# Optimization experiments

Measured on AMD Instinct MI355X. Metric: run time of the kernel, lower is better.

Reference implementation:

```python
import jax, jax.numpy as jnp
import numpy as np

RHO = 10.0
TAU = 0.1


def setup_inputs() -> dict:
    key = jax.random.key(0)
    k1, k2 = jax.random.split(key)
    N, D, C = 8192, 512, 128
    embeddings = jax.random.normal(k1, (N, D), dtype=jnp.float32)
    classes = jax.random.randint(k2, (N,), 0, C, dtype=jnp.int64)
    return {"embeddings": embeddings, "classes": classes}


def reference(embeddings, classes):
    n = embeddings.shape[0]
    dt = embeddings.dtype

    # calculate_similarities_pt: cosine similarity (dot products of L2-normalized embeddings)
    norms = jnp.linalg.norm(embeddings, axis=1, keepdims=True)
    normed = embeddings / jnp.maximum(norms, jnp.asarray(1e-12, dt))
    dot_products = jnp.einsum("nd,md->nm", normed, normed)  # [N, N]

    # calculate_groups_pt: same-class mask (excluding self) and different-class mask
    eq = classes[:, None] == classes[None, :]
    eye = jnp.eye(n, dtype=bool)
    same_group = (eq & ~eye).astype(dt)       # [N, N]
    different_group = (~eq).astype(dt)        # [N, N]

    # diagonal gets factor -RHO -> strongly negative score, effectively masked out
    raw_scores = ((same_group + different_group) * (1.0 + RHO) - RHO) * dot_products / TAU
    max_raw_score = jnp.max(raw_scores, axis=1, keepdims=True)
    shifted_scores = jnp.exp(raw_scores - max_raw_score)

    shifted_positive_scores = same_group * shifted_scores
    sum_shifted_negative_scores = jnp.sum(different_group * shifted_scores, axis=1, keepdims=True)

    denom = shifted_positive_scores + sum_shifted_negative_scores
    # safe_division: 0 where denominator is 0
    ratio = jnp.where(denom > 0, shifted_positive_scores / jnp.where(denom > 0, denom, 1.0), 0.0)
    # safe_log: 0 where argument is 0 (masked by same_group anyway)
    log_ratio = jnp.where(ratio > 0, jnp.log(jnp.where(ratio > 0, ratio, 1.0)), 0.0)
    infonce_losses = -log_ratio * same_group

    num_pos = jnp.sum(same_group)
    loss = jnp.where(num_pos > 0, jnp.sum(infonce_losses) / jnp.where(num_pos > 0, num_pos, 1.0), 0.0)
    return loss
```

## Files before the change

### kernel.cpp

```cpp
#include <hip/hip_runtime.h>
#include <hip/hip_bf16.h>


constexpr int   D      = 512;
constexpr int   BT     = 128;
constexpr int   BK     = 128;
constexpr int   NSTEP  = D / BK;
constexpr float SHIFTL = 14.4269504088896340f;
constexpr float QS2L   = 10.0f * 1.4426950408889634f / 16129.0f;
constexpr float LN2    = 0.6931471805599453f;

typedef __attribute__((ext_vector_type(4))) int i32x4;
typedef unsigned char uchar;
typedef unsigned long ulong_t;

__device__ inline void gload_lds16(const uchar* g, void* l) {
    __builtin_amdgcn_global_load_lds(
        (const __attribute__((address_space(1))) void*)g,
        (__attribute__((address_space(3))) void*)l, 16, 0, 0);
}

__global__ void k_normalize(const float* __restrict__ emb,
                            const int* __restrict__ classes,
                            uchar* __restrict__ normed,
                            int* __restrict__ hist, int n) {
    if (blockIdx.x == 0) {
        __shared__ int h[128];
        if (threadIdx.x < 128) h[threadIdx.x] = 0;
        __syncthreads();
        for (int i = threadIdx.x; i < n; i += 256)
            atomicAdd(&h[classes[i] & 127], 1);
        __syncthreads();
        if (threadIdx.x < 128) hist[threadIdx.x] = h[threadIdx.x];
    }
    int row  = blockIdx.x * 4 + (threadIdx.x >> 6);
    int lane = threadIdx.x & 63;
    if (row >= n) return;
    const float4* src = (const float4*)(emb + (size_t)row * D);
    float4 a = src[lane * 2];
    float4 b = src[lane * 2 + 1];
    float ss = a.x*a.x + a.y*a.y + a.z*a.z + a.w*a.w
             + b.x*b.x + b.y*b.y + b.z*b.z + b.w*b.w;
#pragma unroll
    for (int m = 1; m < 64; m <<= 1) ss += __shfl_xor(ss, m, 64);
    float sc = 127.0f / fmaxf(sqrtf(ss), 1e-12f);
    union { signed char c[8]; ulong_t u; } o;
    float v[8] = {a.x, a.y, a.z, a.w, b.x, b.y, b.z, b.w};
#pragma unroll
    for (int k = 0; k < 8; ++k) {
        int q = (int)rintf(v[k] * sc);
        q = q > 127 ? 127 : (q < -127 ? -127 : q);
        o.c[k] = (signed char)q;
    }
    *(ulong_t*)&normed[(size_t)row * D + lane * 8] = o.u;
}

__global__ __launch_bounds__(256, 2) void k_zgemm(
    const uchar* __restrict__ normed, const int* __restrict__ classes,
    float* __restrict__ Zpart, int n, int nb, int npairs) {
    __shared__ char ring[2][32768];
    __shared__ int clsrow[BT], clscol[BT];

    const int tid  = threadIdx.x;
    const int lane = tid & 63;
    const int w    = tid >> 6;
    const int wm   = w >> 1, wn = w & 1;
    const int l15  = lane & 15, l4 = lane >> 4;
    const size_t QS = (size_t)64 * n;

    int q8 = npairs >> 3, r8 = npairs & 7;
    int xcd = blockIdx.x & 7, off = blockIdx.x >> 3;
    int orig = (xcd < r8 ? xcd * (q8 + 1) : r8 * (q8 + 1) + (xcd - r8) * q8) + off;

    const int sgrid = nb >> 3;
    int idx = orig, si = 0;
    for (;;) { int rc = 36 + (sgrid - 1 - si) * 64; if (idx < rc) break; idx -= rc; ++si; }
    int bi, bj;
    if (idx < 36) { int u = 0, rem = 8; while (idx >= rem) { idx -= rem; ++u; --rem; }
                    bi = si * 8 + u; bj = si * 8 + u + idx; }
    else { idx -= 36; int sj = si + 1 + (idx >> 6); int v = idx & 63;
           bi = si * 8 + (v >> 3); bj = sj * 8 + (v & 7); }
    const int row0 = bi * BT, c0 = bj * BT;
    const bool diagblk = (bi == bj);

    if (tid < BT) clsrow[tid] = classes[row0 + tid];
    else          clscol[tid - BT] = classes[c0 + tid - BT];
    int crow[16];
#pragma unroll
    for (int t = 0; t < 16; ++t)
        crow[t] = classes[row0 + wm * 64 + (t >> 2) * 16 + l4 * 4 + (t & 3)];

    const int src16 = (lane & 3) ^ ((lane >> 3) & 3);
    size_t gA[2], gB[2]; int lo[2];
#pragma unroll
    for (int it = 0; it < 2; ++it) {
        int chunk = w * 2 + it;
        int row   = chunk * 16 + (lane >> 2);
        gA[it] = (size_t)(row0 + row) * D + src16 * 16;
        gB[it] = (size_t)(c0   + row) * D + src16 * 16;
        lo[it] = chunk * 1024;
    }
    char* ringb = &ring[0][0];

    auto STAGE = [&](int sbo, int kk) {
#pragma unroll
        for (int h = 0; h < 2; ++h) {
            int kh = kk + h * 64;
            int so = sbo + h * 16384;
#pragma unroll
            for (int it = 0; it < 2; ++it) {
                gload_lds16(normed + gA[it] + kh, ringb + so + lo[it]);
                gload_lds16(normed + gB[it] + kh, ringb + so + 8192 + lo[it]);
            }
        }
    };

    i32x4 acc[4][4];
#pragma unroll
    for (int a = 0; a < 4; ++a)
#pragma unroll
        for (int b = 0; b < 4; ++b) acc[a][b] = (i32x4){0, 0, 0, 0};

    STAGE(0, 0);
    __builtin_amdgcn_sched_barrier(0);
    asm volatile("s_waitcnt vmcnt(0) lgkmcnt(0)" ::: "memory");
    __builtin_amdgcn_s_barrier();
    __builtin_amdgcn_sched_barrier(0);

    const int rsw = (l15 >> 1) & 3;

#pragma unroll
    for (int kt = 0; kt < NSTEP; ++kt) {
        const int cur = kt & 1;
        if (kt + 1 < NSTEP) STAGE((cur ^ 1) * 32768, (kt + 1) * BK);
        const char* base = ringb + cur * 32768;
        i32x4 af[2][4], bfr[2][4];
#pragma unroll
        for (int h = 0; h < 2; ++h) {
            const char* la = base + h * 16384;
            const char* lb = la + 8192;
#pragma unroll
            for (int mf = 0; mf < 4; ++mf) {
                int ra = wm * 64 + mf * 16 + l15;
                af[h][mf] = *(const i32x4*)(la + ra * 64 + ((l4 ^ rsw) << 4));
            }
#pragma unroll
            for (int nf = 0; nf < 4; ++nf) {
                int rb = wn * 64 + nf * 16 + l15;
                bfr[h][nf] = *(const i32x4*)(lb + rb * 64 + ((l4 ^ rsw) << 4));
            }
        }
        __builtin_amdgcn_s_setprio(1);
#pragma unroll
        for (int h = 0; h < 2; ++h)
#pragma unroll
            for (int mf = 0; mf < 4; ++mf)
#pragma unroll
                for (int nf = 0; nf < 4; ++nf)
                    acc[mf][nf] = __builtin_amdgcn_mfma_i32_16x16x64_i8(
                        af[h][mf], bfr[h][nf], acc[mf][nf], 0, 0, 0);
        __builtin_amdgcn_s_setprio(0);
        __builtin_amdgcn_sched_barrier(0);
        if (kt + 1 < NSTEP) {
            asm volatile("s_waitcnt vmcnt(0)" ::: "memory");
            __builtin_amdgcn_s_barrier();
            __builtin_amdgcn_sched_barrier(0);
        }
    }
    __syncthreads();

    float cqz[4] = {0,0,0,0}, cqn[4] = {0,0,0,0}, cqp[4] = {0,0,0,0};
    float* redr = (float*)ringb;
    float* redc = (float*)(ringb + 16384);

#pragma unroll
    for (int mf = 0; mf < 4; ++mf) {
#pragma unroll
        for (int r = 0; r < 4; ++r) {
            int rr = wm * 64 + mf * 16 + l4 * 4 + r;
            int rg = row0 + rr;
            int cr = crow[mf * 4 + r];
            float z = 0.f, ns = 0.f, p1 = 0.f;
#pragma unroll
            for (int nf = 0; nf < 4; ++nf) {
                int cc = wn * 64 + nf * 16 + l15;
                float t = fmaf((float)acc[mf][nf][r], QS2L, -SHIFTL);
                float e = exp2f(t);
                bool same = (cr == clscol[cc]);
                bool dg   = (rg == c0 + cc);
                if (!same) { z += e; cqz[nf] += e; }
                else if (!dg) { ns += t; p1 += e; cqn[nf] += t; cqp[nf] += e; }
            }
#pragma unroll
            for (int m = 1; m < 16; m <<= 1) {
                z  += __shfl_xor(z,  m, 16);
                ns += __shfl_xor(ns, m, 16);
                p1 += __shfl_xor(p1, m, 16);
            }
            if (l15 == 0) {
                float* p = &redr[(wn * 128 + rr) * 3];
                p[0] = z; p[1] = ns; p[2] = p1;
            }
        }
    }
    if (!diagblk) {
#pragma unroll
        for (int nf = 0; nf < 4; ++nf) {
            float z = cqz[nf], nsv = cqn[nf], p = cqp[nf];
            z += __shfl_xor(z, 16, 64);  z += __shfl_xor(z, 32, 64);
            nsv += __shfl_xor(nsv, 16, 64); nsv += __shfl_xor(nsv, 32, 64);
            p += __shfl_xor(p, 16, 64);  p += __shfl_xor(p, 32, 64);
            if (l4 == 0) {
                float* pp = &redc[(wm * 128 + wn * 64 + nf * 16 + l15) * 3];
                pp[0] = z; pp[1] = nsv; pp[2] = p;
            }
        }
    }
    __syncthreads();

    if (tid < BT) {
#pragma unroll
        for (int q = 0; q < 3; ++q)
            Zpart[q * QS + (size_t)bj * n + row0 + tid] =
                redr[(0 * 128 + tid) * 3 + q] + redr[(1 * 128 + tid) * 3 + q];
    } else if (!diagblk) {
        int cc = tid - BT;
#pragma unroll
        for (int q = 0; q < 3; ++q)
            Zpart[q * QS + (size_t)bi * n + c0 + cc] =
                redc[(0 * 128 + cc) * 3 + q] + redc[(1 * 128 + cc) * 3 + q];
    }
}

__global__ void k_rowterms(const float* __restrict__ Zpart,
                           const int* __restrict__ classes,
                           const int* __restrict__ hist,
                           float* __restrict__ rowloss,
                           float* __restrict__ rowcnt, int n) {
    int i = blockIdx.x * 256 + threadIdx.x;
    if (i >= n) return;
    const size_t QS = (size_t)64 * n;
    float z = 0.f, ns = 0.f, p1 = 0.f;
    for (int s = 0; s < 64; ++s) {
        size_t o = (size_t)s * n + i;
        z  += Zpart[o];
        ns += Zpart[QS + o];
        p1 += Zpart[2 * QS + o];
    }
    float c = (float)(hist[classes[i] & 127] - 1);
    rowloss[i] = -ns * LN2 + c * logf(z) + p1 / z;
    rowcnt[i]  = c;
}

__global__ void k_final(const float* __restrict__ rowloss,
                        const float* __restrict__ rowcnt,
                        float* __restrict__ out, int n) {
    __shared__ float sl[1024];
    __shared__ float sc[1024];
    float l = 0.f, c = 0.f;
    for (int i = threadIdx.x; i < n; i += 1024) {
        l += rowloss[i];
        c += rowcnt[i];
    }
    sl[threadIdx.x] = l;
    sc[threadIdx.x] = c;
    __syncthreads();
    for (int s = 512; s > 0; s >>= 1) {
        if (threadIdx.x < s) {
            sl[threadIdx.x] += sl[threadIdx.x + s];
            sc[threadIdx.x] += sc[threadIdx.x + s];
        }
        __syncthreads();
    }
    if (threadIdx.x == 0)
        out[0] = (sc[0] > 0.f) ? sl[0] / sc[0] : 0.f;
}

extern "C" void kernel_launch(void* const* d_in, const int* in_sizes, int n_in,
                              void* d_out, int out_size, void* d_ws, size_t ws_size,
                              hipStream_t stream) {
    const float* emb     = (const float*)d_in[0];
    const int*   classes = (const int*)d_in[1];
    float*       out     = (float*)d_out;
    const int n  = in_sizes[1];
    const int nb = n / BT;
    const int npairs = nb * (nb + 1) / 2;

    uchar*  normed  = (uchar*)d_ws;
    float*  Zpart   = (float*)((char*)d_ws + (size_t)n * D);
    float*  rowloss = Zpart + (size_t)3 * 64 * n;
    float*  rowcnt  = rowloss + n;
    int*    hist    = (int*)(rowcnt + n);

    k_normalize<<<n / 4, 256, 0, stream>>>(emb, classes, normed, hist, n);
    k_zgemm<<<npairs, 256, 0, stream>>>(normed, classes, Zpart, n, nb, npairs);
    k_rowterms<<<(n + 255) / 256, 256, 0, stream>>>(Zpart, classes, hist, rowloss, rowcnt, n);
    k_final<<<1, 1024, 0, stream>>>(rowloss, rowcnt, out, n);
}
```

Measured before the change: 89.13 us.

## Process two column tiles per block with triple-buffered 64-wide K pipeline

Each workgroup now computes a 128x256 strip (one row tile against two adjacent column tiles), reusing the A fragments across both B tiles and halving the block count. The K loop is split into 64-byte steps with a three-slot LDS ring and partial vmcnt waits, so loads run two stages ahead of the MFMAs. The block mapping drops the supertile XCD-locality ordering for a simple row-major pair walk and hardcodes 1056 blocks and 64 row tiles. It doubles the accumulator registers, which may reduce occupancy, and leaves odd tails where a block handles only one tile.

```diff
diff --git a/kernel.cpp b/kernel.cpp
--- a/kernel.cpp
+++ b/kernel.cpp
@@ -4,7 +4,7 @@
 
 constexpr int   D      = 512;
 constexpr int   BT     = 128;
-constexpr int   BK     = 128;
+constexpr int   BK     = 64;
 constexpr int   NSTEP  = D / BK;
 constexpr float SHIFTL = 14.4269504088896340f;
 constexpr float QS2L   = 10.0f * 1.4426950408889634f / 16129.0f;
@@ -57,9 +57,9 @@
 
 __global__ __launch_bounds__(256, 2) void k_zgemm(
     const uchar* __restrict__ normed, const int* __restrict__ classes,
-    float* __restrict__ Zpart, int n, int nb, int npairs) {
-    __shared__ char ring[2][32768];
-    __shared__ int clsrow[BT], clscol[BT];
+    float* __restrict__ Zpart, int n, int nblk) {
+    __shared__ char ring[3][24576];
+    __shared__ int clsrow[BT], clscol1[BT], clscol2[BT];
 
     const int tid  = threadIdx.x;
     const int lane = tid & 63;
@@ -68,62 +68,63 @@
     const int l15  = lane & 15, l4 = lane >> 4;
     const size_t QS = (size_t)64 * n;
 
-    int q8 = npairs >> 3, r8 = npairs & 7;
+    int q8 = nblk >> 3, r8 = nblk & 7;
     int xcd = blockIdx.x & 7, off = blockIdx.x >> 3;
     int orig = (xcd < r8 ? xcd * (q8 + 1) : r8 * (q8 + 1) + (xcd - r8) * q8) + off;
 
-    const int sgrid = nb >> 3;
-    int idx = orig, si = 0;
-    for (;;) { int rc = 36 + (sgrid - 1 - si) * 64; if (idx < rc) break; idx -= rc; ++si; }
-    int bi, bj;
-    if (idx < 36) { int u = 0, rem = 8; while (idx >= rem) { idx -= rem; ++u; --rem; }
-                    bi = si * 8 + u; bj = si * 8 + u + idx; }
-    else { idx -= 36; int sj = si + 1 + (idx >> 6); int v = idx & 63;
-           bi = si * 8 + (v >> 3); bj = sj * 8 + (v & 7); }
-    const int row0 = bi * BT, c0 = bj * BT;
-    const bool diagblk = (bi == bj);
-
-    if (tid < BT) clsrow[tid] = classes[row0 + tid];
-    else          clscol[tid - BT] = classes[c0 + tid - BT];
+    int idx = orig, bi = 0;
+    for (;;) { int npb = (64 - bi + 1) >> 1; if (idx < npb) break; idx -= npb; ++bi; }
+    const int  bj1    = bi + idx * 2;
+    const bool valid2 = (bj1 + 1 < 64);
+    const int  bj2    = valid2 ? bj1 + 1 : bj1;
+    const int  row0 = bi * BT, c01 = bj1 * BT, c02 = bj2 * BT;
+    const bool diag1 = (bj1 == bi);
+
+    if (tid < BT) {
+        clsrow[tid]  = classes[row0 + tid];
+        clscol2[tid] = classes[c02 + tid];
+    } else {
+        clscol1[tid - BT] = classes[c01 + tid - BT];
+    }
     int crow[16];
 #pragma unroll
     for (int t = 0; t < 16; ++t)
         crow[t] = classes[row0 + wm * 64 + (t >> 2) * 16 + l4 * 4 + (t & 3)];
 
     const int src16 = (lane & 3) ^ ((lane >> 3) & 3);
-    size_t gA[2], gB[2]; int lo[2];
+    size_t gA[2], gB1[2], gB2[2]; int lo[2];
 #pragma unroll
     for (int it = 0; it < 2; ++it) {
         int chunk = w * 2 + it;
         int row   = chunk * 16 + (lane >> 2);
-        gA[it] = (size_t)(row0 + row) * D + src16 * 16;
-        gB[it] = (size_t)(c0   + row) * D + src16 * 16;
-        lo[it] = chunk * 1024;
+        gA[it]  = (size_t)(row0 + row) * D + src16 * 16;
+        gB1[it] = (size_t)(c01  + row) * D + src16 * 16;
+        gB2[it] = (size_t)(c02  + row) * D + src16 * 16;
+        lo[it]  = chunk * 1024;
     }
     char* ringb = &ring[0][0];
 
     auto STAGE = [&](int sbo, int kk) {
 #pragma unroll
-        for (int h = 0; h < 2; ++h) {
-            int kh = kk + h * 64;
-            int so = sbo + h * 16384;
-#pragma unroll
-            for (int it = 0; it < 2; ++it) {
-                gload_lds16(normed + gA[it] + kh, ringb + so + lo[it]);
-                gload_lds16(normed + gB[it] + kh, ringb + so + 8192 + lo[it]);
-            }
+        for (int it = 0; it < 2; ++it) {
+            gload_lds16(normed + gA[it]  + kk, ringb + sbo + lo[it]);
+            gload_lds16(normed + gB1[it] + kk, ringb + sbo + 8192  + lo[it]);
+            gload_lds16(normed + gB2[it] + kk, ringb + sbo + 16384 + lo[it]);
         }
     };
 
-    i32x4 acc[4][4];
-#pragma unroll
-    for (int a = 0; a < 4; ++a)
-#pragma unroll
-        for (int b = 0; b < 4; ++b) acc[a][b] = (i32x4){0, 0, 0, 0};
+    i32x4 acc[2][4][4];
+#pragma unroll
+    for (int t = 0; t < 2; ++t)
+#pragma unroll
+        for (int a = 0; a < 4; ++a)
+#pragma unroll
+            for (int b = 0; b < 4; ++b) acc[t][a][b] = (i32x4){0, 0, 0, 0};
 
     STAGE(0, 0);
+    STAGE(24576, BK);
     __builtin_amdgcn_sched_barrier(0);
-    asm volatile("s_waitcnt vmcnt(0) lgkmcnt(0)" ::: "memory");
+    asm volatile("s_waitcnt vmcnt(6) lgkmcnt(0)" ::: "memory");
     __builtin_amdgcn_s_barrier();
     __builtin_amdgcn_sched_barrier(0);
 
@@ -131,104 +132,114 @@
 
 #pragma unroll
     for (int kt = 0; kt < NSTEP; ++kt) {
-        const int cur = kt & 1;
-        if (kt + 1 < NSTEP) STAGE((cur ^ 1) * 32768, (kt + 1) * BK);
-        const char* base = ringb + cur * 32768;
-        i32x4 af[2][4], bfr[2][4];
-#pragma unroll
-        for (int h = 0; h < 2; ++h) {
-            const char* la = base + h * 16384;
-            const char* lb = la + 8192;
-#pragma unroll
-            for (int mf = 0; mf < 4; ++mf) {
-                int ra = wm * 64 + mf * 16 + l15;
-                af[h][mf] = *(const i32x4*)(la + ra * 64 + ((l4 ^ rsw) << 4));
+        const int cur = kt % 3;
+        if (kt + 2 < NSTEP) STAGE(((kt + 2) % 3) * 24576, (kt + 2) * BK);
+        const char* la  = ringb + cur * 24576;
+        const char* lb1 = la + 8192;
+        const char* lb2 = la + 16384;
+        i32x4 af[4], b1[4], b2[4];
+#pragma unroll
+        for (int mf = 0; mf < 4; ++mf) {
+            int ra = wm * 64 + mf * 16 + l15;
+            af[mf] = *(const i32x4*)(la + ra * 64 + ((l4 ^ rsw) << 4));
+        }
+#pragma unroll
+        for (int nf = 0; nf < 4; ++nf) {
+            int rb = wn * 64 + nf * 16 + l15;
+            int ro = rb * 64 + ((l4 ^ rsw) << 4);
+            b1[nf] = *(const i32x4*)(lb1 + ro);
+            b2[nf] = *(const i32x4*)(lb2 + ro);
+        }
+        __builtin_amdgcn_s_setprio(1);
+#pragma unroll
+        for (int mf = 0; mf < 4; ++mf)
+#pragma unroll
+            for (int nf = 0; nf < 4; ++nf) {
+                acc[0][mf][nf] = __builtin_amdgcn_mfma_i32_16x16x64_i8(
+                    af[mf], b1[nf], acc[0][mf][nf], 0, 0, 0);
+                acc[1][mf][nf] = __builtin_amdgcn_mfma_i32_16x16x64_i8(
+                    af[mf], b2[nf], acc[1][mf][nf], 0, 0, 0);
             }
-#pragma unroll
-            for (int nf = 0; nf < 4; ++nf) {
-                int rb = wn * 64 + nf * 16 + l15;
-                bfr[h][nf] = *(const i32x4*)(lb + rb * 64 + ((l4 ^ rsw) << 4));
-            }
-        }
-        __builtin_amdgcn_s_setprio(1);
-#pragma unroll
-        for (int h = 0; h < 2; ++h)
-#pragma unroll
-            for (int mf = 0; mf < 4; ++mf)
-#pragma unroll
-                for (int nf = 0; nf < 4; ++nf)
-                    acc[mf][nf] = __builtin_amdgcn_mfma_i32_16x16x64_i8(
-                        af[h][mf], bfr[h][nf], acc[mf][nf], 0, 0, 0);
         __builtin_amdgcn_s_setprio(0);
         __builtin_amdgcn_sched_barrier(0);
+        if (kt + 2 < NSTEP)       asm volatile("s_waitcnt vmcnt(6)" ::: "memory");
+        else if (kt + 2 == NSTEP) asm volatile("s_waitcnt vmcnt(0)" ::: "memory");
         if (kt + 1 < NSTEP) {
-            asm volatile("s_waitcnt vmcnt(0)" ::: "memory");
             __builtin_amdgcn_s_barrier();
             __builtin_amdgcn_sched_barrier(0);
         }
     }
     __syncthreads();
 
-    float cqz[4] = {0,0,0,0}, cqn[4] = {0,0,0,0}, cqp[4] = {0,0,0,0};
     float* redr = (float*)ringb;
-    float* redc = (float*)(ringb + 16384);
-
-#pragma unroll
-    for (int mf = 0; mf < 4; ++mf) {
-#pragma unroll
-        for (int r = 0; r < 4; ++r) {
-            int rr = wm * 64 + mf * 16 + l4 * 4 + r;
-            int rg = row0 + rr;
-            int cr = crow[mf * 4 + r];
-            float z = 0.f, ns = 0.f, p1 = 0.f;
+    float* redc = (float*)(ringb + 8192);
+
+#pragma unroll
+    for (int t = 0; t < 2; ++t) {
+        if (t == 1 && !valid2) break;
+        const int  c0t   = t ? c02 : c01;
+        const int  bjt   = t ? bj2 : bj1;
+        const int* clsc  = t ? clscol2 : clscol1;
+        const bool dgblk = (t == 0) && diag1;
+
+        float cqz[4] = {0,0,0,0}, cqn[4] = {0,0,0,0}, cqp[4] = {0,0,0,0};
+#pragma unroll
+        for (int mf = 0; mf < 4; ++mf) {
+#pragma unroll
+            for (int r = 0; r < 4; ++r) {
+                int rr = wm * 64 + mf * 16 + l4 * 4 + r;
+                int cr = crow[mf * 4 + r];
+                float z = 0.f, ns = 0.f, p1 = 0.f;
+#pragma unroll
+                for (int nf = 0; nf < 4; ++nf) {
+                    int cc = wn * 64 + nf * 16 + l15;
+                    float tt = fmaf((float)acc[t][mf][nf][r], QS2L, -SHIFTL);
+                    float e = exp2f(tt);
+                    bool same = (cr == clsc[cc]);
+                    bool dg   = dgblk && (rr == cc);
+                    if (!same) { z += e; cqz[nf] += e; }
+                    else if (!dg) { ns += tt; p1 += e; cqn[nf] += tt; cqp[nf] += e; }
+                }
+#pragma unroll
+                for (int m = 1; m < 16; m <<= 1) {
+                    z  += __shfl_xor(z,  m, 16);
+                    ns += __shfl_xor(ns, m, 16);
+                    p1 += __shfl_xor(p1, m, 16);
+                }
+                if (l15 == 0) {
+                    float* p = &redr[(wn * 128 + rr) * 3];
+                    p[0] = z; p[1] = ns; p[2] = p1;
+                }
+            }
+        }
+        if (!dgblk) {
 #pragma unroll
             for (int nf = 0; nf < 4; ++nf) {
-                int cc = wn * 64 + nf * 16 + l15;
-                float t = fmaf((float)acc[mf][nf][r], QS2L, -SHIFTL);
-                float e = exp2f(t);
-                bool same = (cr == clscol[cc]);
-                bool dg   = (rg == c0 + cc);
-                if (!same) { z += e; cqz[nf] += e; }
-                else if (!dg) { ns += t; p1 += e; cqn[nf] += t; cqp[nf] += e; }
+                float z = cqz[nf], nsv = cqn[nf], p = cqp[nf];
+                z += __shfl_xor(z, 16, 64);  z += __shfl_xor(z, 32, 64);
+                nsv += __shfl_xor(nsv, 16, 64); nsv += __shfl_xor(nsv, 32, 64);
+                p += __shfl_xor(p, 16, 64);  p += __shfl_xor(p, 32, 64);
+                if (l4 == 0) {
+                    float* pp = &redc[(wm * 128 + wn * 64 + nf * 16 + l15) * 3];
+                    pp[0] = z; pp[1] = nsv; pp[2] = p;
+                }
             }
-#pragma unroll
-            for (int m = 1; m < 16; m <<= 1) {
-                z  += __shfl_xor(z,  m, 16);
-                ns += __shfl_xor(ns, m, 16);
-                p1 += __shfl_xor(p1, m, 16);
-            }
-            if (l15 == 0) {
-                float* p = &redr[(wn * 128 + rr) * 3];
-                p[0] = z; p[1] = ns; p[2] = p1;
-            }
-        }
-    }
-    if (!diagblk) {
-#pragma unroll
-        for (int nf = 0; nf < 4; ++nf) {
-            float z = cqz[nf], nsv = cqn[nf], p = cqp[nf];
-            z += __shfl_xor(z, 16, 64);  z += __shfl_xor(z, 32, 64);
-            nsv += __shfl_xor(nsv, 16, 64); nsv += __shfl_xor(nsv, 32, 64);
-            p += __shfl_xor(p, 16, 64);  p += __shfl_xor(p, 32, 64);
-            if (l4 == 0) {
-                float* pp = &redc[(wm * 128 + wn * 64 + nf * 16 + l15) * 3];
-                pp[0] = z; pp[1] = nsv; pp[2] = p;
-            }
-        }
-    }
-    __syncthreads();
-
-    if (tid < BT) {
-#pragma unroll
-        for (int q = 0; q < 3; ++q)
-            Zpart[q * QS + (size_t)bj * n + row0 + tid] =
-                redr[(0 * 128 + tid) * 3 + q] + redr[(1 * 128 + tid) * 3 + q];
-    } else if (!diagblk) {
-        int cc = tid - BT;
-#pragma unroll
-        for (int q = 0; q < 3; ++q)
-            Zpart[q * QS + (size_t)bi * n + c0 + cc] =
-                redc[(0 * 128 + cc) * 3 + q] + redc[(1 * 128 + cc) * 3 + q];
+        }
+        __syncthreads();
+
+        if (tid < BT) {
+#pragma unroll
+            for (int q = 0; q < 3; ++q)
+                Zpart[q * QS + (size_t)bjt * n + row0 + tid] =
+                    redr[(0 * 128 + tid) * 3 + q] + redr[(1 * 128 + tid) * 3 + q];
+        } else if (!dgblk) {
+            int cc = tid - BT;
+#pragma unroll
+            for (int q = 0; q < 3; ++q)
+                Zpart[q * QS + (size_t)bi * n + c0t + cc] =
+                    redc[(0 * 128 + cc) * 3 + q] + redc[(1 * 128 + cc) * 3 + q];
+        }
+        __syncthreads();
     }
 }
 
@@ -282,9 +293,8 @@
     const float* emb     = (const float*)d_in[0];
     const int*   classes = (const int*)d_in[1];
     float*       out     = (float*)d_out;
-    const int n  = in_sizes[1];
-    const int nb = n / BT;
-    const int npairs = nb * (nb + 1) / 2;
+    const int n = in_sizes[1];
+    const int nblk = 1056;
 
     uchar*  normed  = (uchar*)d_ws;
     float*  Zpart   = (float*)((char*)d_ws + (size_t)n * D);
@@ -293,7 +303,7 @@
     int*    hist    = (int*)(rowcnt + n);
 
     k_normalize<<<n / 4, 256, 0, stream>>>(emb, classes, normed, hist, n);
-    k_zgemm<<<npairs, 256, 0, stream>>>(normed, classes, Zpart, n, nb, npairs);
+    k_zgemm<<<nblk, 256, 0, stream>>>(normed, classes, Zpart, n, nblk);
     k_rowterms<<<(n + 255) / 256, 256, 0, stream>>>(Zpart, classes, hist, rowloss, rowcnt, n);
     k_final<<<1, 1024, 0, stream>>>(rowloss, rowcnt, out, n);
 }
```

Result: slower. 93.77 us (+5.2%).

## Hold A fragments in registers and stage the full-K B tile in LDS

Applied to the files above, without the earlier changes.

The int8 similarity GEMM drops the double-buffered K-loop, which staged both A and B through LDS. Each wave now loads its 32 rows of A straight from global memory into registers across the whole K=512. The 128-column B tile is copied into a 64KB swizzled LDS buffer in one pass, followed by a single barrier. Waves now split by rows only, so each wave covers all 128 columns; this removes the cross-wave row reduction but needs a four-way column-partial reduction. The cost is that global loads no longer overlap with MFMA work inside a block, and the kernel uses more registers for A and the larger accumulator set.

```diff
diff --git a/kernel.cpp b/kernel.cpp
--- a/kernel.cpp
+++ b/kernel.cpp
@@ -4,8 +4,6 @@
 
 constexpr int   D      = 512;
 constexpr int   BT     = 128;
-constexpr int   BK     = 128;
-constexpr int   NSTEP  = D / BK;
 constexpr float SHIFTL = 14.4269504088896340f;
 constexpr float QS2L   = 10.0f * 1.4426950408889634f / 16129.0f;
 constexpr float LN2    = 0.6931471805599453f;
@@ -58,13 +56,12 @@
 __global__ __launch_bounds__(256, 2) void k_zgemm(
     const uchar* __restrict__ normed, const int* __restrict__ classes,
     float* __restrict__ Zpart, int n, int nb, int npairs) {
-    __shared__ char ring[2][32768];
+    __shared__ char Blds[65536];
     __shared__ int clsrow[BT], clscol[BT];
 
     const int tid  = threadIdx.x;
     const int lane = tid & 63;
     const int w    = tid >> 6;
-    const int wm   = w >> 1, wn = w & 1;
     const int l15  = lane & 15, l4 = lane >> 4;
     const size_t QS = (size_t)64 * n;
 
@@ -85,111 +82,83 @@
 
     if (tid < BT) clsrow[tid] = classes[row0 + tid];
     else          clscol[tid - BT] = classes[c0 + tid - BT];
-    int crow[16];
-#pragma unroll
-    for (int t = 0; t < 16; ++t)
-        crow[t] = classes[row0 + wm * 64 + (t >> 2) * 16 + l4 * 4 + (t & 3)];
-
-    const int src16 = (lane & 3) ^ ((lane >> 3) & 3);
-    size_t gA[2], gB[2]; int lo[2];
-#pragma unroll
-    for (int it = 0; it < 2; ++it) {
-        int chunk = w * 2 + it;
-        int row   = chunk * 16 + (lane >> 2);
-        gA[it] = (size_t)(row0 + row) * D + src16 * 16;
-        gB[it] = (size_t)(c0   + row) * D + src16 * 16;
-        lo[it] = chunk * 1024;
-    }
-    char* ringb = &ring[0][0];
-
-    auto STAGE = [&](int sbo, int kk) {
-#pragma unroll
-        for (int h = 0; h < 2; ++h) {
-            int kh = kk + h * 64;
-            int so = sbo + h * 16384;
-#pragma unroll
-            for (int it = 0; it < 2; ++it) {
-                gload_lds16(normed + gA[it] + kh, ringb + so + lo[it]);
-                gload_lds16(normed + gB[it] + kh, ringb + so + 8192 + lo[it]);
-            }
-        }
-    };
-
-    i32x4 acc[4][4];
-#pragma unroll
-    for (int a = 0; a < 4; ++a)
-#pragma unroll
-        for (int b = 0; b < 4; ++b) acc[a][b] = (i32x4){0, 0, 0, 0};
-
-    STAGE(0, 0);
-    __builtin_amdgcn_sched_barrier(0);
-    asm volatile("s_waitcnt vmcnt(0) lgkmcnt(0)" ::: "memory");
-    __builtin_amdgcn_s_barrier();
-    __builtin_amdgcn_sched_barrier(0);
-
-    const int rsw = (l15 >> 1) & 3;
-
-#pragma unroll
-    for (int kt = 0; kt < NSTEP; ++kt) {
-        const int cur = kt & 1;
-        if (kt + 1 < NSTEP) STAGE((cur ^ 1) * 32768, (kt + 1) * BK);
-        const char* base = ringb + cur * 32768;
-        i32x4 af[2][4], bfr[2][4];
-#pragma unroll
-        for (int h = 0; h < 2; ++h) {
-            const char* la = base + h * 16384;
-            const char* lb = la + 8192;
-#pragma unroll
-            for (int mf = 0; mf < 4; ++mf) {
-                int ra = wm * 64 + mf * 16 + l15;
-                af[h][mf] = *(const i32x4*)(la + ra * 64 + ((l4 ^ rsw) << 4));
-            }
-#pragma unroll
-            for (int nf = 0; nf < 4; ++nf) {
-                int rb = wn * 64 + nf * 16 + l15;
-                bfr[h][nf] = *(const i32x4*)(lb + rb * 64 + ((l4 ^ rsw) << 4));
-            }
-        }
-        __builtin_amdgcn_s_setprio(1);
-#pragma unroll
-        for (int h = 0; h < 2; ++h)
-#pragma unroll
-            for (int mf = 0; mf < 4; ++mf)
-#pragma unroll
-                for (int nf = 0; nf < 4; ++nf)
-                    acc[mf][nf] = __builtin_amdgcn_mfma_i32_16x16x64_i8(
-                        af[h][mf], bfr[h][nf], acc[mf][nf], 0, 0, 0);
-        __builtin_amdgcn_s_setprio(0);
-        __builtin_amdgcn_sched_barrier(0);
-        if (kt + 1 < NSTEP) {
-            asm volatile("s_waitcnt vmcnt(0)" ::: "memory");
-            __builtin_amdgcn_s_barrier();
-            __builtin_amdgcn_sched_barrier(0);
-        }
-    }
-    __syncthreads();
-
-    float cqz[4] = {0,0,0,0}, cqn[4] = {0,0,0,0}, cqp[4] = {0,0,0,0};
-    float* redr = (float*)ringb;
-    float* redc = (float*)(ringb + 16384);
-
-#pragma unroll
-    for (int mf = 0; mf < 4; ++mf) {
+
+    int crow[2][4];
+#pragma unroll
+    for (int rg = 0; rg < 2; ++rg)
+#pragma unroll
+        for (int r = 0; r < 4; ++r)
+            crow[rg][r] = classes[row0 + w * 32 + rg * 16 + l4 * 4 + r];
+    int ccv[8];
+#pragma unroll
+    for (int cf = 0; cf < 8; ++cf)
+        ccv[cf] = classes[c0 + cf * 16 + l15];
+
+    i32x4 areg[2][8];
+#pragma unroll
+    for (int rg = 0; rg < 2; ++rg)
+#pragma unroll
+        for (int kf = 0; kf < 8; ++kf)
+            areg[rg][kf] = *(const i32x4*)&normed[
+                (size_t)(row0 + w * 32 + rg * 16 + l15) * D + kf * 64 + l4 * 16];
+
+    {
+        const int colw = w * 2 + (lane >> 5);
+        const int p    = lane & 31;
+#pragma unroll
+        for (int rr = 0; rr < 16; ++rr) {
+            int col = rr * 8 + colw;
+            gload_lds16(&normed[(size_t)(c0 + col) * D + ((p ^ (col & 7)) << 4)],
+                        Blds + (rr * 8 + w * 2) * 512 + lane * 16);
+        }
+    }
+    __syncthreads();
+
+    i32x4 acc[2][8];
+#pragma unroll
+    for (int rg = 0; rg < 2; ++rg)
+#pragma unroll
+        for (int cf = 0; cf < 8; ++cf) acc[rg][cf] = (i32x4){0, 0, 0, 0};
+
+    const int csw = l15 & 7;
+#pragma unroll
+    for (int kf = 0; kf < 8; ++kf) {
+#pragma unroll
+        for (int cf = 0; cf < 8; ++cf) {
+            int cc = cf * 16 + l15;
+            i32x4 bf = *(const i32x4*)(Blds + cc * 512 +
+                        (((kf * 4 + l4) ^ csw) << 4));
+            acc[0][cf] = __builtin_amdgcn_mfma_i32_16x16x64_i8(
+                areg[0][kf], bf, acc[0][cf], 0, 0, 0);
+            acc[1][cf] = __builtin_amdgcn_mfma_i32_16x16x64_i8(
+                areg[1][kf], bf, acc[1][cf], 0, 0, 0);
+        }
+    }
+    __syncthreads();
+
+    float* redc = (float*)Blds;
+    float* redr = (float*)(Blds + 8192);
+
+    float cq[8][3];
+#pragma unroll
+    for (int cf = 0; cf < 8; ++cf) cq[cf][0] = cq[cf][1] = cq[cf][2] = 0.f;
+
+#pragma unroll
+    for (int rg = 0; rg < 2; ++rg) {
 #pragma unroll
         for (int r = 0; r < 4; ++r) {
-            int rr = wm * 64 + mf * 16 + l4 * 4 + r;
-            int rg = row0 + rr;
-            int cr = crow[mf * 4 + r];
+            int rr = w * 32 + rg * 16 + l4 * 4 + r;
+            int cr = crow[rg][r];
             float z = 0.f, ns = 0.f, p1 = 0.f;
 #pragma unroll
-            for (int nf = 0; nf < 4; ++nf) {
-                int cc = wn * 64 + nf * 16 + l15;
-                float t = fmaf((float)acc[mf][nf][r], QS2L, -SHIFTL);
-                float e = exp2f(t);
-                bool same = (cr == clscol[cc]);
-                bool dg   = (rg == c0 + cc);
-                if (!same) { z += e; cqz[nf] += e; }
-                else if (!dg) { ns += t; p1 += e; cqn[nf] += t; cqp[nf] += e; }
+            for (int cf = 0; cf < 8; ++cf) {
+                int cc = cf * 16 + l15;
+                float tt = fmaf((float)acc[rg][cf][r], QS2L, -SHIFTL);
+                float e = exp2f(tt);
+                bool same = (cr == ccv[cf]);
+                bool dg   = diagblk && (rr == cc);
+                if (!same) { z += e; cq[cf][0] += e; }
+                else if (!dg) { ns += tt; p1 += e; cq[cf][1] += tt; cq[cf][2] += e; }
             }
 #pragma unroll
             for (int m = 1; m < 16; m <<= 1) {
@@ -198,20 +167,21 @@
                 p1 += __shfl_xor(p1, m, 16);
             }
             if (l15 == 0) {
-                float* p = &redr[(wn * 128 + rr) * 3];
-                p[0] = z; p[1] = ns; p[2] = p1;
+                redr[rr * 3 + 0] = z;
+                redr[rr * 3 + 1] = ns;
+                redr[rr * 3 + 2] = p1;
             }
         }
     }
     if (!diagblk) {
 #pragma unroll
-        for (int nf = 0; nf < 4; ++nf) {
-            float z = cqz[nf], nsv = cqn[nf], p = cqp[nf];
+        for (int cf = 0; cf < 8; ++cf) {
+            float z = cq[cf][0], nsv = cq[cf][1], p = cq[cf][2];
             z += __shfl_xor(z, 16, 64);  z += __shfl_xor(z, 32, 64);
             nsv += __shfl_xor(nsv, 16, 64); nsv += __shfl_xor(nsv, 32, 64);
             p += __shfl_xor(p, 16, 64);  p += __shfl_xor(p, 32, 64);
             if (l4 == 0) {
-                float* pp = &redc[(wm * 128 + wn * 64 + nf * 16 + l15) * 3];
+                float* pp = &redc[(w * 128 + cf * 16 + l15) * 3];
                 pp[0] = z; pp[1] = nsv; pp[2] = p;
             }
         }
@@ -221,14 +191,14 @@
     if (tid < BT) {
 #pragma unroll
         for (int q = 0; q < 3; ++q)
-            Zpart[q * QS + (size_t)bj * n + row0 + tid] =
-                redr[(0 * 128 + tid) * 3 + q] + redr[(1 * 128 + tid) * 3 + q];
+            Zpart[q * QS + (size_t)bj * n + row0 + tid] = redr[tid * 3 + q];
     } else if (!diagblk) {
         int cc = tid - BT;
 #pragma unroll
         for (int q = 0; q < 3; ++q)
             Zpart[q * QS + (size_t)bi * n + c0 + cc] =
-                redc[(0 * 128 + cc) * 3 + q] + redc[(1 * 128 + cc) * 3 + q];
+                redc[(0 * 128 + cc) * 3 + q] + redc[(1 * 128 + cc) * 3 + q] +
+                redc[(2 * 128 + cc) * 3 + q] + redc[(3 * 128 + cc) * 3 + q];
     }
 }
 
```

Result: faster. 86.46 us (-3.0%).
